# Optimization experiments

Hardware: AMD Instinct MI355X
Metric: run time of the kernel (lower is better)

Reference implementation:

```python
import jax, jax.numpy as jnp
import numpy as np

HEAD_DIM = 72
NUM_HEADS = 16
EPS = 1e-6
ROPE_THETA = 10000.0


def _rms_norm(x, scale):
    # normalize over last dim in fp32, apply learned scale
    xf = x.astype(jnp.float32)
    normed = xf * jax.lax.rsqrt(jnp.mean(xf * xf, axis=-1, keepdims=True) + EPS)
    return (normed * scale.astype(jnp.float32)).astype(x.dtype)


def _rope_cos_sin(pixel_position_ids, dtype):
    # pixel_position_ids: [B, N, 2] -> cos/sin [B, N, head_dim]
    dim = HEAD_DIM // 2                      # 36
    inv_freq = 1.0 / (ROPE_THETA ** (jnp.arange(0, dim, 2, dtype=jnp.float32) / dim))  # [18]
    pos = pixel_position_ids.astype(jnp.float32)          # [B, N, 2]
    freqs = pos[..., None] * inv_freq                      # [B, N, 2, 18]
    emb = jnp.concatenate([freqs, freqs], axis=-1)         # [B, N, 2, 36]
    cos = jnp.cos(emb)
    sin = jnp.sin(emb)
    # concat x-axis and y-axis halves -> [B, N, 72]
    cos = cos.reshape(cos.shape[0], cos.shape[1], -1)
    sin = sin.reshape(sin.shape[0], sin.shape[1], -1)
    return cos.astype(dtype), sin.astype(dtype)


def _rotate_half(x):
    half = x.shape[-1] // 2
    return jnp.concatenate([-x[..., half:], x[..., :half]], axis=-1)


def _apply_2d_rope(x, cos, sin):
    # x: [B, N, H, Dh]; cos/sin: [B, N, Dh] split into 2 spatial halves of 36 channels each
    cpd = 2 * (x.shape[-1] // 4)             # channels_per_dim = 36
    outs = []
    for k in range(2):
        xk = x[..., k * cpd:(k + 1) * cpd]
        ck = cos[:, :, None, k * cpd:(k + 1) * cpd]   # broadcast over heads (unsqueeze_dim=2)
        sk = sin[:, :, None, k * cpd:(k + 1) * cpd]
        outs.append(xk * ck + _rotate_half(xk) * sk)
    return jnp.concatenate(outs, axis=-1)


def reference(hidden_states, pixel_position_ids, Wq, Wk, Wv, Wo, q_scale, k_scale, v_scale):
    B, N, D = hidden_states.shape
    H, Dh = NUM_HEADS, HEAD_DIM
    scaling = Dh ** -0.5

    q = (hidden_states @ Wq).reshape(B, N, H, Dh)
    k = (hidden_states @ Wk).reshape(B, N, H, Dh)
    v = (hidden_states @ Wv).reshape(B, N, H, Dh)

    q = _rms_norm(q, q_scale)
    k = _rms_norm(k, k_scale)
    v = _rms_norm(v, v_scale)

    cos, sin = _rope_cos_sin(pixel_position_ids, hidden_states.dtype)
    q = _apply_2d_rope(q, cos, sin)
    k = _apply_2d_rope(k, cos, sin)

    # full softmax attention: [B, H, N, N]
    attn = jnp.einsum('bnhd,bmhd->bhnm', q, k) * scaling
    attn = jax.nn.softmax(attn, axis=-1)
    out = jnp.einsum('bhnm,bmhd->bnhd', attn, v).reshape(B, N, H * Dh)
    return out @ Wo


def setup_inputs() -> dict:
    key = jax.random.key(0)
    k1, k2, k3, k4, k5, k6 = jax.random.split(key, 6)
    B, N, D = 8, 1024, 1152
    grid = 32  # 448 / 14
    return {
        'hidden_states': jax.random.normal(k1, (B, N, D), dtype=jnp.float32),
        'pixel_position_ids': jax.random.randint(k2, (B, N, 2), 0, grid, dtype=jnp.int32),
        'Wq': jax.random.normal(k3, (D, D), dtype=jnp.float32) * 0.02,
        'Wk': jax.random.normal(k4, (D, D), dtype=jnp.float32) * 0.02,
        'Wv': jax.random.normal(k5, (D, D), dtype=jnp.float32) * 0.02,
        'Wo': jax.random.normal(k6, (D, D), dtype=jnp.float32) * 0.02,
        'q_scale': jnp.ones((HEAD_DIM,), dtype=jnp.float32),
        'k_scale': jnp.ones((HEAD_DIM,), dtype=jnp.float32),
        'v_scale': jnp.ones((HEAD_DIM,), dtype=jnp.float32),
    }
```

## Files before the change

### kernel.cpp

```cpp
#include <hip/hip_runtime.h>
#include <hip/hip_bf16.h>

typedef unsigned short u16;
typedef __attribute__((ext_vector_type(8))) short bf16x8;
typedef __attribute__((ext_vector_type(8))) unsigned short u16x8;
typedef __attribute__((ext_vector_type(4))) float f32x4;

#define NTOK 8192
#define DMODEL 1152
#define NHEAD 16
#define DHEAD 72
#define DPAD 96
#define VROWS 80
#define NQKV 3456

__device__ __forceinline__ u16 f2bf(float f){
  __hip_bfloat16 h = __float2bfloat16(f);
  return *reinterpret_cast<u16*>(&h);
}
__device__ __forceinline__ float bf2f(u16 u){
  union { unsigned int i; float f; } v; v.i = ((unsigned int)u) << 16; return v.f;
}
__device__ __forceinline__ void gload16(const void* g, void* l){
  __builtin_amdgcn_global_load_lds((const __attribute__((address_space(1))) void*)g,
                                   (__attribute__((address_space(3))) void*)l, 16, 0, 0);
}

__global__ __launch_bounds__(256) void cvt_x(const float* __restrict__ X, u16* __restrict__ Xb){
  int i = (blockIdx.x * 256 + threadIdx.x) * 8;
  float4 a = *(const float4*)(X + i);
  float4 b = *(const float4*)(X + i + 4);
  u16x8 o;
  o[0]=f2bf(a.x); o[1]=f2bf(a.y); o[2]=f2bf(a.z); o[3]=f2bf(a.w);
  o[4]=f2bf(b.x); o[5]=f2bf(b.y); o[6]=f2bf(b.z); o[7]=f2bf(b.w);
  *(u16x8*)(Xb + i) = o;
}

__global__ __launch_bounds__(256) void pack_w(const float* __restrict__ Wq, const float* __restrict__ Wk,
                                              const float* __restrict__ Wv, const float* __restrict__ Wo,
                                              u16* __restrict__ WT){
  __shared__ u16 t[32][33];
  int tx = threadIdx.x & 31, ty = threadIdx.x >> 5;
  int k0 = blockIdx.x * 32, n0 = blockIdx.y * 32;
  int ng = n0 + tx;
  const float* W; int nl;
  if (ng < 1152)      { W = Wq; nl = ng; }
  else if (ng < 2304) { W = Wk; nl = ng - 1152; }
  else if (ng < 3456) { W = Wv; nl = ng - 2304; }
  else                { W = Wo; nl = ng - 3456; }
  #pragma unroll
  for (int i = 0; i < 4; i++)
    t[ty + i*8][tx] = f2bf(W[(size_t)(k0 + ty + i*8) * 1152 + nl]);
  __syncthreads();
  #pragma unroll
  for (int i = 0; i < 4; i++)
    WT[(size_t)(n0 + ty + i*8) * 1152 + k0 + tx] = t[tx][ty + i*8];
}

__global__ __launch_bounds__(256) void rope_tab(const int* __restrict__ pid,
                                                float* __restrict__ tc, float* __restrict__ ts){
  int i = blockIdx.x * 256 + threadIdx.x;
  if (i >= NTOK * 36) return;
  int tok = i / 36, r = i - tok * 36;
  int c = r / 18, j = r - c * 18;
  float freq = exp2f(-0.7382062433f * (float)j);
  float ang = (float)pid[tok * 2 + c] * freq;
  float s, co;
  sincosf(ang, &s, &co);
  tc[i] = co; ts[i] = s;
}

template<int FP32OUT>
__global__ __launch_bounds__(256) void gemm_bt(const u16* __restrict__ A, const u16* __restrict__ Bt,
                                               void* __restrict__ C, int Ncols){
  __shared__ u16 Al[128 * 64];
  __shared__ u16 Bl[128 * 64];
  int tid = threadIdx.x, lane = tid & 63, w = tid >> 6;
  int wr = w >> 1, wc = w & 1, l16 = lane & 15, lq = lane >> 4;
  int m0 = blockIdx.x * 128, n0 = blockIdx.y * 128;
  f32x4 acc[4][4] = {};
  int grow = lane >> 3;
  int gchunk = (lane & 7) ^ grow;
  const char* Abase = (const char*)A  + (size_t)(m0 + grow) * 2304 + gchunk * 16;
  const char* Bbase = (const char*)Bt + (size_t)(n0 + grow) * 2304 + gchunk * 16;
  int sw = l16 & 7;
  for (int kt = 0; kt < 18; ++kt){
    __syncthreads();
    #pragma unroll
    for (int i = 0; i < 4; i++){
      int j = w * 4 + i;
      gload16(Abase + (size_t)j * 8 * 2304 + kt * 128, &Al[j * 512]);
      gload16(Bbase + (size_t)j * 8 * 2304 + kt * 128, &Bl[j * 512]);
    }
    __syncthreads();
    #pragma unroll
    for (int kk = 0; kk < 2; kk++){
      bf16x8 af[4], bfr[4];
      #pragma unroll
      for (int m = 0; m < 4; m++){
        int row = wr * 64 + m * 16 + l16;
        af[m] = *(const bf16x8*)&Al[row * 64 + (((kk * 4 + lq) ^ sw) * 8)];
      }
      #pragma unroll
      for (int n = 0; n < 4; n++){
        int row = wc * 64 + n * 16 + l16;
        bfr[n] = *(const bf16x8*)&Bl[row * 64 + (((kk * 4 + lq) ^ sw) * 8)];
      }
      #pragma unroll
      for (int m = 0; m < 4; m++)
        #pragma unroll
        for (int n = 0; n < 4; n++)
          acc[m][n] = __builtin_amdgcn_mfma_f32_16x16x32_bf16(af[m], bfr[n], acc[m][n], 0, 0, 0);
    }
  }
  #pragma unroll
  for (int m = 0; m < 4; m++)
    #pragma unroll
    for (int n = 0; n < 4; n++)
      #pragma unroll
      for (int r = 0; r < 4; r++){
        int row = m0 + wr * 64 + m * 16 + lq * 4 + r;
        int col = n0 + wc * 64 + n * 16 + l16;
        if (FP32OUT) ((float*)C)[(size_t)row * Ncols + col] = acc[m][n][r];
        else         ((u16*)  C)[(size_t)row * Ncols + col] = f2bf(acc[m][n][r]);
      }
}

__global__ __launch_bounds__(256) void rmsrope(const u16* __restrict__ QKV,
    const float* __restrict__ tc, const float* __restrict__ ts,
    const float* __restrict__ qsc, const float* __restrict__ ksc, const float* __restrict__ vsc,
    u16* __restrict__ Qp, u16* __restrict__ Kp, u16* __restrict__ Vt){
  __shared__ u16 vl[72][264];
  int h = blockIdx.y, tid = threadIdx.x;
  int tok = blockIdx.x * 256 + tid;
  int b = tok >> 10, n = tok & 1023;
  int n0 = (blockIdx.x & 3) * 256;
  int bh = b * NHEAD + h;
  const u16* base = QKV + (size_t)tok * NQKV + h * DHEAD;

  {
    u16x8 vr[9];
    #pragma unroll
    for (int i = 0; i < 9; i++) vr[i] = *(const u16x8*)(base + 2304 + i * 8);
    float ss = 0.f;
    #pragma unroll
    for (int i = 0; i < 9; i++)
      #pragma unroll
      for (int e = 0; e < 8; e++){ float f = bf2f(vr[i][e]); ss += f * f; }
    float rv = rsqrtf(ss * (1.f / 72.f) + 1e-6f);
    #pragma unroll
    for (int i = 0; i < 9; i++)
      #pragma unroll
      for (int e = 0; e < 8; e++){
        int d = i * 8 + e;
        vl[d][tid] = f2bf(bf2f(vr[i][e]) * rv * vsc[d]);
      }
  }
  #pragma unroll
  for (int qk = 0; qk < 2; ++qk){
    const u16* src = base + qk * 1152;
    const float* sc = qk ? ksc : qsc;
    u16* dst = qk ? Kp : Qp;
    float fold = qk ? 1.0f : 0.17002219f;
    u16x8 xr[9];
    #pragma unroll
    for (int i = 0; i < 9; i++) xr[i] = *(const u16x8*)(src + i * 8);
    float ss = 0.f;
    #pragma unroll
    for (int i = 0; i < 9; i++)
      #pragma unroll
      for (int e = 0; e < 8; e++){ float f = bf2f(xr[i][e]); ss += f * f; }
    float rs_ = rsqrtf(ss * (1.f / 72.f) + 1e-6f);
    float x[72];
    #pragma unroll
    for (int i = 0; i < 9; i++)
      #pragma unroll
      for (int e = 0; e < 8; e++){ int d = i * 8 + e; x[d] = bf2f(xr[i][e]) * rs_ * sc[d]; }
    #pragma unroll
    for (int c = 0; c < 2; c++)
      #pragma unroll
      for (int j = 0; j < 18; j++){
        float co = tc[(size_t)tok * 36 + c * 18 + j];
        float si = ts[(size_t)tok * 36 + c * 18 + j];
        float x1 = x[c * 36 + j], x2 = x[c * 36 + j + 18];
        x[c * 36 + j]      = x1 * co - x2 * si;
        x[c * 36 + j + 18] = x2 * co + x1 * si;
      }
    size_t off = ((size_t)bh * 1024 + n) * DPAD;
    #pragma unroll
    for (int i = 0; i < 9; i++){
      u16x8 o;
      #pragma unroll
      for (int e = 0; e < 8; e++) o[e] = f2bf(x[i * 8 + e] * fold);
      *(u16x8*)(dst + off + i * 8) = o;
    }
    u16x8 z = {0,0,0,0,0,0,0,0};
    #pragma unroll
    for (int i = 9; i < 12; i++) *(u16x8*)(dst + off + i * 8) = z;
  }
  __syncthreads();
  u16x8 z = {0,0,0,0,0,0,0,0};
  u16x8 on = {0x3F80,0x3F80,0x3F80,0x3F80,0x3F80,0x3F80,0x3F80,0x3F80};
  for (int c = tid; c < VROWS * 32; c += 256){
    int row = c >> 5, seg = c & 31;
    u16x8 v;
    if (row < 72)       v = *(const u16x8*)&vl[row][seg * 8];
    else if (row == 72) v = on;
    else                v = z;
    *(u16x8*)(Vt + ((size_t)bh * VROWS + row) * 1024 + n0 + seg * 8) = v;
  }
}

__global__ __launch_bounds__(512, 4) void attn(const u16* __restrict__ Qp, const u16* __restrict__ Kp,
                                               const u16* __restrict__ Vt, u16* __restrict__ AO){
  __shared__ u16 Kl[64][104];
  __shared__ u16 Vl[VROWS][72];
  __shared__ u16 Pl[8][32][72];
  int tid = threadIdx.x, lane = tid & 63, w = tid >> 6;
  int l16 = lane & 15, lq = lane >> 4;
  int bh = blockIdx.y, b = bh >> 4, h = bh & 15;
  int q0 = blockIdx.x * 256;
  const u16* Qb = Qp + (size_t)bh * 1024 * DPAD;
  const u16* Kb = Kp + (size_t)bh * 1024 * DPAD;
  const u16* Vb = Vt + (size_t)bh * VROWS * 1024;

  bf16x8 qf[2][3];
  #pragma unroll
  for (int mt = 0; mt < 2; mt++)
    #pragma unroll
    for (int ks = 0; ks < 3; ks++)
      qf[mt][ks] = *(const bf16x8*)(Qb + (size_t)(q0 + w * 32 + mt * 16 + l16) * DPAD + ks * 32 + lq * 8);

  f32x4 accO[2][5] = {};

  for (int kv = 0; kv < 16; ++kv){
    __syncthreads();
    for (int c = tid; c < 768; c += 512){
      int row = c / 12, col = c - row * 12;
      *(u16x8*)&Kl[row][col * 8] = *(const u16x8*)(Kb + (size_t)(kv * 64 + row) * DPAD + col * 8);
    }
    for (int c = tid; c < VROWS * 8; c += 512){
      int row = c >> 3, seg = c & 7;
      *(u16x8*)&Vl[row][seg * 8] = *(const u16x8*)(Vb + (size_t)row * 1024 + kv * 64 + seg * 8);
    }
    __syncthreads();

    f32x4 accS[2][4] = {};
    #pragma unroll
    for (int j = 0; j < 4; j++)
      #pragma unroll
      for (int ks = 0; ks < 3; ks++){
        bf16x8 kf = *(const bf16x8*)&Kl[j * 16 + l16][ks * 32 + lq * 8];
        accS[0][j] = __builtin_amdgcn_mfma_f32_16x16x32_bf16(qf[0][ks], kf, accS[0][j], 0, 0, 0);
        accS[1][j] = __builtin_amdgcn_mfma_f32_16x16x32_bf16(qf[1][ks], kf, accS[1][j], 0, 0, 0);
      }
    #pragma unroll
    for (int mt = 0; mt < 2; mt++)
      #pragma unroll
      for (int j = 0; j < 4; j++)
        #pragma unroll
        for (int r = 0; r < 4; r++)
          Pl[w][mt * 16 + lq * 4 + r][j * 16 + l16] = f2bf(exp2f(accS[mt][j][r]));
    #pragma unroll
    for (int ks = 0; ks < 2; ks++){
      bf16x8 pf0 = *(const bf16x8*)&Pl[w][l16][ks * 32 + lq * 8];
      bf16x8 pf1 = *(const bf16x8*)&Pl[w][16 + l16][ks * 32 + lq * 8];
      #pragma unroll
      for (int nf = 0; nf < 5; nf++){
        bf16x8 vf = *(const bf16x8*)&Vl[nf * 16 + l16][ks * 32 + lq * 8];
        accO[0][nf] = __builtin_amdgcn_mfma_f32_16x16x32_bf16(pf0, vf, accO[0][nf], 0, 0, 0);
        accO[1][nf] = __builtin_amdgcn_mfma_f32_16x16x32_bf16(pf1, vf, accO[1][nf], 0, 0, 0);
      }
    }
  }
  #pragma unroll
  for (int mt = 0; mt < 2; mt++)
    #pragma unroll
    for (int r = 0; r < 4; r++){
      float s = __shfl(accO[mt][4][r], (lane & 48) + 8);
      float inv = 1.f / s;
      int qg = q0 + w * 32 + mt * 16 + lq * 4 + r;
      size_t rowoff = ((size_t)(b * 1024 + qg)) * DMODEL + h * DHEAD;
      #pragma unroll
      for (int nf = 0; nf < 5; nf++){
        int d = nf * 16 + l16;
        if (d < 72) AO[rowoff + d] = f2bf(accO[mt][nf][r] * inv);
      }
    }
}

extern "C" void kernel_launch(void* const* d_in, const int* in_sizes, int n_in,
                              void* d_out, int out_size, void* d_ws, size_t ws_size,
                              hipStream_t stream){
  const float* X   = (const float*)d_in[0];
  const int*   pid = (const int*)  d_in[1];
  const float* Wq  = (const float*)d_in[2];
  const float* Wk  = (const float*)d_in[3];
  const float* Wv  = (const float*)d_in[4];
  const float* Wo  = (const float*)d_in[5];
  const float* qsc = (const float*)d_in[6];
  const float* ksc = (const float*)d_in[7];
  const float* vsc = (const float*)d_in[8];
  char* ws = (char*)d_ws;
  u16*   Xb  = (u16*)(ws);
  u16*   WT  = (u16*)(ws + 18874368);
  u16*   QKV = (u16*)(ws + 29491200);
  u16*   Qp  = (u16*)(ws + 86114304);
  u16*   Kp  = (u16*)(ws + 111280128);
  u16*   Vt  = (u16*)(ws + 136445952);
  float* tc  = (float*)(ws + 157417472);
  float* tsn = (float*)(ws + 158597120);
  u16*   AO  = QKV;

  cvt_x  <<<4608, 256, 0, stream>>>(X, Xb);
  pack_w <<<dim3(36, 144), 256, 0, stream>>>(Wq, Wk, Wv, Wo, WT);
  rope_tab<<<1152, 256, 0, stream>>>(pid, tc, tsn);
  gemm_bt<0><<<dim3(64, 27), 256, 0, stream>>>(Xb, WT, QKV, 3456);
  rmsrope<<<dim3(32, 16), 256, 0, stream>>>(QKV, tc, tsn, qsc, ksc, vsc, Qp, Kp, Vt);
  attn   <<<dim3(4, 128), 512, 0, stream>>>(Qp, Kp, Vt, AO);
  gemm_bt<1><<<dim3(64, 9), 256, 0, stream>>>(AO, WT + (size_t)3456 * 1152, d_out, 1152);
}
```

Measured before the change: 375.0 us.

## Replace QKV projection GEMM with 256x256-tile, 8-wave, double-buffered MFMA kernel

Adds a new gemm256 kernel for the QKV projection. It uses 256x256 output tiles, 512 threads (8 waves) and a 128 KB LDS ping-pong buffer. Global-to-LDS loads for the next K chunk are interleaved with MFMA quads, using explicit vmcnt/lgkmcnt waits, barriers and setprio, and a grouped block-index swizzle is added for L2 locality. The aim is more data reuse per LDS load and better overlap of memory traffic with compute than the previous 128x128 kernel. The cost is padded work on the last column tile (3456 is not a multiple of 256) and a more fragile hand-scheduled pipeline.

```diff
diff --git a/kernel.cpp b/kernel.cpp
--- a/kernel.cpp
+++ b/kernel.cpp
@@ -25,6 +25,13 @@
   __builtin_amdgcn_global_load_lds((const __attribute__((address_space(1))) void*)g,
                                    (__attribute__((address_space(3))) void*)l, 16, 0, 0);
 }
+
+#define FENCE asm volatile("" ::: "memory")
+#define BARX() do{ FENCE; __builtin_amdgcn_s_barrier(); FENCE; }while(0)
+#define LGK0 asm volatile("s_waitcnt lgkmcnt(0)" ::: "memory")
+#define VMW(N) asm volatile("s_waitcnt vmcnt(" #N ")" ::: "memory")
+#define PRIO1 __builtin_amdgcn_s_setprio(1)
+#define PRIO0 __builtin_amdgcn_s_setprio(0)
 
 __global__ __launch_bounds__(256) void cvt_x(const float* __restrict__ X, u16* __restrict__ Xb){
   int i = (blockIdx.x * 256 + threadIdx.x) * 8;
@@ -68,6 +75,114 @@
   float s, co;
   sincosf(ang, &s, &co);
   tc[i] = co; ts[i] = s;
+}
+
+#define REG(b,idx) ((b)*32768 + (idx)*8192)
+
+__device__ __forceinline__ void stage_half(const char* g, u16* lreg, int w, int lane){
+  #pragma unroll
+  for (int j = 0; j < 2; j++){
+    int row = j*64 + w*8 + (lane >> 3);
+    int chunk = (lane & 7) ^ (row & 7);
+    gload16(g + (size_t)row*2304 + chunk*16, (char*)lreg + j*8192 + w*1024);
+  }
+}
+__device__ __forceinline__ void rdA(bf16x8 (&d)[4][2], const u16* L, int b, int wm, int mbase, int l16, int lq){
+  #pragma unroll
+  for (int mi = 0; mi < 4; mi++)
+    #pragma unroll
+    for (int kk = 0; kk < 2; kk++){
+      int rl = (mbase + mi)*16 + l16;
+      int byt = (rl*128 + kk*64 + lq*16) ^ ((rl & 7) << 4);
+      d[mi][kk] = *(const bf16x8*)((const char*)L + (size_t)REG(b, wm)*2 + byt);
+    }
+}
+__device__ __forceinline__ void rdB(bf16x8 (&d)[2][2], const u16* L, int b, int wn, int nbase, int l16, int lq){
+  #pragma unroll
+  for (int ni = 0; ni < 2; ni++)
+    #pragma unroll
+    for (int kk = 0; kk < 2; kk++){
+      int rl = (wn & 1)*64 + (nbase + ni)*16 + l16;
+      int byt = (rl*128 + kk*64 + lq*16) ^ ((rl & 7) << 4);
+      d[ni][kk] = *(const bf16x8*)((const char*)L + (size_t)REG(b, 2 + (wn >> 1))*2 + byt);
+    }
+}
+template<int MB, int NB>
+__device__ __forceinline__ void quad(f32x4 (&acc)[8][4], const bf16x8 (&aa)[4][2], const bf16x8 (&bb)[2][2]){
+  #pragma unroll
+  for (int mi = 0; mi < 4; mi++)
+    #pragma unroll
+    for (int ni = 0; ni < 2; ni++)
+      #pragma unroll
+      for (int kk = 0; kk < 2; kk++)
+        acc[MB+mi][NB+ni] = __builtin_amdgcn_mfma_f32_16x16x32_bf16(aa[mi][kk], bb[ni][kk], acc[MB+mi][NB+ni], 0, 0, 0);
+}
+
+__global__ __launch_bounds__(512, 2) void gemm256(const u16* __restrict__ A, const u16* __restrict__ Bt,
+                                                  u16* __restrict__ C){
+  __shared__ u16 L[65536];
+  int tid = threadIdx.x, lane = tid & 63, w = tid >> 6;
+  int wm = w >> 2, wn = w & 3;
+  int l16 = lane & 15, lq = lane >> 4;
+  int bid = blockIdx.x;
+  int swz = (bid & 7) * 56 + (bid >> 3);
+  int m0 = (swz & 31) * 256, n0 = (swz >> 5) * 256;
+  const char* Ab = (const char*)A  + (size_t)m0 * 2304;
+  const char* Bb = (const char*)Bt + (size_t)n0 * 2304;
+  f32x4 acc[8][4] = {};
+  bf16x8 a[4][2], a2[4][2], b0[2][2], b1[2][2];
+
+  stage_half(Ab,                          L + REG(0,0), w, lane);
+  stage_half(Ab + (size_t)128*2304,       L + REG(0,1), w, lane);
+  stage_half(Bb,                          L + REG(0,2), w, lane);
+  stage_half(Bb + (size_t)128*2304,       L + REG(0,3), w, lane);
+  stage_half(Bb + 128,                    L + REG(1,2), w, lane);
+  stage_half(Bb + (size_t)128*2304 + 128, L + REG(1,3), w, lane);
+  VMW(4); BARX();
+
+  #pragma unroll 1
+  for (int i = 0; i < 9; ++i){
+    bool pf = (i < 8);
+    size_t k1 = (size_t)(2*i+1)*128, k2 = (size_t)(2*i+2)*128, k3 = (size_t)(2*i+3)*128;
+    rdA(a,  L, 0, wm, 0, l16, lq);
+    rdB(b0, L, 0, wn, 0, l16, lq);
+    stage_half(Ab + k1, L + REG(1,0), w, lane);
+    BARX(); LGK0; PRIO1; quad<0,0>(acc, a, b0); PRIO0; BARX();
+    rdB(b1, L, 0, wn, 2, l16, lq);
+    stage_half(Ab + (size_t)128*2304 + k1, L + REG(1,1), w, lane);
+    BARX(); LGK0; PRIO1; quad<0,2>(acc, a, b1); PRIO0; BARX();
+    rdA(a2, L, 0, wm, 4, l16, lq);
+    if (pf) stage_half(Bb + k2, L + REG(0,2), w, lane);
+    BARX(); LGK0; PRIO1; quad<4,0>(acc, a2, b0); PRIO0; BARX();
+    if (pf) stage_half(Bb + (size_t)128*2304 + k2, L + REG(0,3), w, lane);
+    BARX(); PRIO1; quad<4,2>(acc, a2, b1); PRIO0;
+    if (pf) { VMW(4); } else { VMW(0); }
+    BARX();
+    rdA(a,  L, 1, wm, 0, l16, lq);
+    rdB(b0, L, 1, wn, 0, l16, lq);
+    if (pf) stage_half(Ab + k2, L + REG(0,0), w, lane);
+    BARX(); LGK0; PRIO1; quad<0,0>(acc, a, b0); PRIO0; BARX();
+    rdB(b1, L, 1, wn, 2, l16, lq);
+    if (pf) stage_half(Ab + (size_t)128*2304 + k2, L + REG(0,1), w, lane);
+    BARX(); LGK0; PRIO1; quad<0,2>(acc, a, b1); PRIO0; BARX();
+    rdA(a2, L, 1, wm, 4, l16, lq);
+    if (pf) stage_half(Bb + k3, L + REG(1,2), w, lane);
+    BARX(); LGK0; PRIO1; quad<4,0>(acc, a2, b0); PRIO0; BARX();
+    if (pf) stage_half(Bb + (size_t)128*2304 + k3, L + REG(1,3), w, lane);
+    BARX(); PRIO1; quad<4,2>(acc, a2, b1); PRIO0;
+    if (pf) { VMW(4); } else { VMW(0); }
+    BARX();
+  }
+  #pragma unroll
+  for (int mi = 0; mi < 8; mi++)
+    #pragma unroll
+    for (int ni = 0; ni < 4; ni++)
+      #pragma unroll
+      for (int r = 0; r < 4; r++){
+        int row = m0 + wm*128 + mi*16 + lq*4 + r;
+        int col = n0 + wn*64 + ni*16 + l16;
+        if (col < NQKV) C[(size_t)row * NQKV + col] = f2bf(acc[mi][ni][r]);
+      }
 }
 
 template<int FP32OUT>
@@ -315,7 +430,7 @@
   cvt_x  <<<4608, 256, 0, stream>>>(X, Xb);
   pack_w <<<dim3(36, 144), 256, 0, stream>>>(Wq, Wk, Wv, Wo, WT);
   rope_tab<<<1152, 256, 0, stream>>>(pid, tc, tsn);
-  gemm_bt<0><<<dim3(64, 27), 256, 0, stream>>>(Xb, WT, QKV, 3456);
+  gemm256<<<448, 512, 0, stream>>>(Xb, WT, QKV);
   rmsrope<<<dim3(32, 16), 256, 0, stream>>>(QKV, tc, tsn, qsc, ksc, vsc, Qp, Kp, Vt);
   attn   <<<dim3(4, 128), 512, 0, stream>>>(Qp, Kp, Vt, AO);
   gemm_bt<1><<<dim3(64, 9), 256, 0, stream>>>(AO, WT + (size_t)3456 * 1152, d_out, 1152);
```

Result: faster. 358.0 us (-4.5%).
